# Performance work log

Hardware: AMD Instinct MI355X
Metric: run time of the kernel (lower is better)

## Reference

```python
import jax, jax.numpy as jnp
import numpy as np

D_MODEL = 768
NUM_HEADS = 12
D_K = D_MODEL // NUM_HEADS


def setup_inputs() -> dict:
    key = jax.random.key(0)
    ks = jax.random.split(key, 11)
    B, S = 2, 2048
    s = 1.0 / np.sqrt(D_MODEL)
    inp = {
        'q': jax.random.normal(ks[0], (B, S, D_MODEL), jnp.float32),
        'k': jax.random.normal(ks[1], (B, S, D_MODEL), jnp.float32),
        'v': jax.random.normal(ks[2], (B, S, D_MODEL), jnp.float32),
        'w_q': jax.random.normal(ks[3], (D_MODEL, D_MODEL), jnp.float32) * s,
        'b_q': jnp.zeros((D_MODEL,), jnp.float32),
        'w_k': jax.random.normal(ks[4], (D_MODEL, D_MODEL), jnp.float32) * s,
        'b_k': jnp.zeros((D_MODEL,), jnp.float32),
        'w_v': jax.random.normal(ks[5], (D_MODEL, D_MODEL), jnp.float32) * s,
        'b_v': jnp.zeros((D_MODEL,), jnp.float32),
        'w_o': jax.random.normal(ks[6], (D_MODEL, D_MODEL), jnp.float32) * s,
        'b_o': jnp.zeros((D_MODEL,), jnp.float32),
    }
    return inp


def _split_heads(x):
    # (B, S, D) -> (B, H, S, d_k)
    B, S, _ = x.shape
    return x.reshape(B, S, NUM_HEADS, D_K).transpose(0, 2, 1, 3)


def reference(q, k, v, w_q, b_q, w_k, b_k, w_v, b_v, w_o, b_o):
    qh = _split_heads(q @ w_q + b_q)
    kh = _split_heads(k @ w_k + b_k)
    vh = _split_heads(v @ w_v + b_v)
    scale = 1.0 / jnp.sqrt(jnp.asarray(D_K, qh.dtype))
    scores = jnp.einsum('bhqd,bhkd->bhqk', qh, kh) * scale  # [B,H,Sq,Sk]
    attn_weights = jax.nn.softmax(scores, axis=-1)
    ctx = jnp.einsum('bhqk,bhkd->bhqd', attn_weights, vh)
    B, H, S, _ = ctx.shape
    ctx = ctx.transpose(0, 2, 1, 3).reshape(B, S, D_MODEL)
    out = ctx @ w_o + b_o  # dropout = identity (eval mode)
    return out, attn_weights
```

## Files before the change

### kernel.cpp

```cpp
#include <hip/hip_runtime.h>
#include <math.h>

#define HH 12
#define SS 2048
#define DM 768
#define DK 64

typedef _Float16 f16x8 __attribute__((ext_vector_type(8)));
typedef _Float16 f16x4 __attribute__((ext_vector_type(4)));
typedef float    f32x4 __attribute__((ext_vector_type(4)));

#define MFMA_F16(A, B, C) __builtin_amdgcn_mfma_f32_16x16x32_f16((A), (B), (C), 0, 0, 0)

__global__ __launch_bounds__(256) void conv_w_kernel(
        const float* __restrict__ w0, const float* __restrict__ w1,
        const float* __restrict__ w2, const float* __restrict__ w3,
        _Float16* hi0, _Float16* lo0, _Float16* hi1, _Float16* lo1,
        _Float16* hi2, _Float16* lo2, _Float16* hi3, _Float16* lo3)
{
    __shared__ float T[64][68];
    const int z = blockIdx.z;
    const float* W = (z == 0) ? w0 : (z == 1) ? w1 : (z == 2) ? w2 : w3;
    _Float16* Whi  = (z == 0) ? hi0 : (z == 1) ? hi1 : (z == 2) ? hi2 : hi3;
    _Float16* Wlo  = (z == 0) ? lo0 : (z == 1) ? lo1 : (z == 2) ? lo2 : lo3;

    const int tid = threadIdx.x;
    const int k0 = blockIdx.y * 64, n0 = blockIdx.x * 64;

    #pragma unroll
    for (int i = 0; i < 4; ++i) {
        int r = (tid >> 4) + i * 16;
        int c = (tid & 15) * 4;
        *(float4*)&T[r][c] = *(const float4*)&W[(size_t)(k0 + r) * DM + n0 + c];
    }
    __syncthreads();

    const int n = tid >> 2, kq = (tid & 3) * 16;
    f16x8 ha, la, hb, lb;
    #pragma unroll
    for (int j = 0; j < 8; ++j) {
        float v = T[kq + j][n];
        _Float16 h = (_Float16)v;
        ha[j] = h; la[j] = (_Float16)(v - (float)h);
    }
    #pragma unroll
    for (int j = 0; j < 8; ++j) {
        float v = T[kq + 8 + j][n];
        _Float16 h = (_Float16)v;
        hb[j] = h; lb[j] = (_Float16)(v - (float)h);
    }
    size_t o = (size_t)(n0 + n) * DM + k0 + kq;
    *(f16x8*)&Whi[o]     = ha;
    *(f16x8*)&Whi[o + 8] = hb;
    *(f16x8*)&Wlo[o]     = la;
    *(f16x8*)&Wlo[o + 8] = lb;
}

template <int MODE>
__global__ __launch_bounds__(256) void gemm16_kernel(
        const float* __restrict__ A, const _Float16* __restrict__ Bhi,
        const _Float16* __restrict__ Blo, const float* __restrict__ bias,
        _Float16* __restrict__ Chi, _Float16* __restrict__ Clo,
        float* __restrict__ Cf)
{
    const int tid  = threadIdx.x;
    const int wave = tid >> 6, lane = tid & 63;
    const int lrow = lane & 15;
    const int lk   = (lane >> 4) * 8;
    const int grow = (lane >> 4) * 4;
    const int n0   = blockIdx.x * 64;
    const int m0   = blockIdx.y * 64;
    const int mr   = m0 + wave * 16 + lrow;

    f32x4 acc[4];
    #pragma unroll
    for (int nf = 0; nf < 4; ++nf) acc[nf] = (f32x4){0.f, 0.f, 0.f, 0.f};

    const float* Arow = A + (size_t)mr * DM;

    #pragma unroll 2
    for (int kt = 0; kt < 24; ++kt) {
        const int k0 = kt * 32 + lk;
        float4 x = *(const float4*)&Arow[k0];
        float4 y = *(const float4*)&Arow[k0 + 4];
        float vv[8] = {x.x, x.y, x.z, x.w, y.x, y.y, y.z, y.w};
        f16x8 ah, al;
        #pragma unroll
        for (int j = 0; j < 8; ++j) {
            _Float16 h = (_Float16)vv[j];
            ah[j] = h; al[j] = (_Float16)(vv[j] - (float)h);
        }
        #pragma unroll
        for (int nf = 0; nf < 4; ++nf) {
            const size_t bo = (size_t)(n0 + nf * 16 + lrow) * DM + k0;
            f16x8 bh_ = *(const f16x8*)&Bhi[bo];
            f16x8 bl_ = *(const f16x8*)&Blo[bo];
            acc[nf] = MFMA_F16(ah, bh_, acc[nf]);
            acc[nf] = MFMA_F16(al, bh_, acc[nf]);
            acc[nf] = MFMA_F16(ah, bl_, acc[nf]);
        }
    }

    float bb[4];
    #pragma unroll
    for (int nf = 0; nf < 4; ++nf) bb[nf] = bias[n0 + nf * 16 + lrow];

    if (MODE == 0) {
        const int h = blockIdx.x;
        #pragma unroll
        for (int nf = 0; nf < 4; ++nf)
            #pragma unroll
            for (int r = 0; r < 4; ++r) {
                int m = m0 + wave * 16 + grow + r;
                int b_ = m >> 11, s_ = m & 2047;
                float v = acc[nf][r] + bb[nf];
                _Float16 h16 = (_Float16)v;
                size_t o = (((size_t)(b_ * HH + h) * SS + s_) << 6) + nf * 16 + lrow;
                Chi[o] = h16;
                Clo[o] = (_Float16)(v - (float)h16);
            }
    } else if (MODE == 1) {
        __shared__ _Float16 T[2][64][72];
        #pragma unroll
        for (int nf = 0; nf < 4; ++nf)
            #pragma unroll
            for (int r = 0; r < 4; ++r) {
                float v = acc[nf][r] + bb[nf];
                _Float16 h16 = (_Float16)v;
                int ml = wave * 16 + grow + r;
                T[0][nf * 16 + lrow][ml] = h16;
                T[1][nf * 16 + lrow][ml] = (_Float16)(v - (float)h16);
            }
        __syncthreads();
        const int h  = blockIdx.x;
        const int b_ = m0 >> 11, s0 = m0 & 2047;
        int row = tid >> 1;
        int p = row >> 6, dk = row & 63, sh = (tid & 1) * 32;
        const _Float16* src = &T[p][dk][sh];
        _Float16* dst = (p ? Clo : Chi) +
                        ((size_t)(b_ * HH + h) * DK + dk) * SS + s0 + sh;
        #pragma unroll
        for (int j = 0; j < 32; j += 8)
            *(f16x8*)&dst[j] = *(const f16x8*)&src[j];
    } else {
        #pragma unroll
        for (int nf = 0; nf < 4; ++nf)
            #pragma unroll
            for (int r = 0; r < 4; ++r) {
                int m = m0 + wave * 16 + grow + r;
                Cf[(size_t)m * DM + n0 + nf * 16 + lrow] = acc[nf][r] + bb[nf];
            }
    }
}

__global__ __launch_bounds__(256) void attn_kernel(
        const _Float16* __restrict__ Qhi, const _Float16* __restrict__ Qlo,
        const _Float16* __restrict__ Khi, const _Float16* __restrict__ Klo,
        const _Float16* __restrict__ Vthi, const _Float16* __restrict__ Vtlo,
        float* __restrict__ attnW, float* __restrict__ ctx)
{
    __shared__ float Ps[4][16][34];

    const int tid  = threadIdx.x;
    const int wave = tid >> 6;
    const int lane = tid & 63;
    const int lrow = lane & 15;
    const int lk   = (lane >> 4) * 8;
    const int grow = (lane >> 4) * 4;

    const int qt = blockIdx.x;
    const int bh = blockIdx.y;
    const int qw0 = qt * 64 + wave * 16;
    const size_t qkbase = (size_t)bh * SS * DK;
    const size_t vbase  = (size_t)bh * DK * SS;

    f16x8 qhi[2], qlo[2];
    {
        const size_t qidx = qkbase + (size_t)(qw0 + lrow) * DK + lk;
        qhi[0] = *(const f16x8*)&Qhi[qidx];
        qhi[1] = *(const f16x8*)&Qhi[qidx + 32];
        qlo[0] = *(const f16x8*)&Qlo[qidx];
        qlo[1] = *(const f16x8*)&Qlo[qidx + 32];
    }

    float lsum[4] = {0.f, 0.f, 0.f, 0.f};
    f32x4 Oacc[4];
    #pragma unroll
    for (int n = 0; n < 4; ++n) Oacc[n] = (f32x4){0.f, 0.f, 0.f, 0.f};

    float (*ps)[34] = Ps[wave];

    for (int kt = 0; kt < 64; ++kt) {
        #pragma unroll
        for (int sub = 0; sub < 2; ++sub) {
            const int k16 = kt * 2 + sub;
            const size_t kidx = qkbase + (size_t)(k16 * 16 + lrow) * DK + lk;
            f16x8 khi0 = *(const f16x8*)&Khi[kidx];
            f16x8 khi1 = *(const f16x8*)&Khi[kidx + 32];
            f16x8 klo0 = *(const f16x8*)&Klo[kidx];
            f16x8 klo1 = *(const f16x8*)&Klo[kidx + 32];
            f32x4 cA = {0.f, 0.f, 0.f, 0.f};
            f32x4 cB = {0.f, 0.f, 0.f, 0.f};
            cA = MFMA_F16(qhi[0], khi0, cA);
            cA = MFMA_F16(qhi[1], khi1, cA);
            cA = MFMA_F16(qlo[0], khi0, cA);
            cB = MFMA_F16(qlo[1], khi1, cB);
            cB = MFMA_F16(qhi[0], klo0, cB);
            cB = MFMA_F16(qhi[1], klo1, cB);
            #pragma unroll
            for (int r = 0; r < 4; ++r) {
                float pv = __expf((cA[r] + cB[r]) * 0.125f);
                lsum[r] += pv;
                attnW[((size_t)bh * SS + qw0 + grow + r) * SS + k16 * 16 + lrow] = pv;
                ps[grow + r][sub * 16 + lrow] = pv * 16.0f;
            }
        }
        float pf[8];
        #pragma unroll
        for (int j = 0; j < 8; ++j) pf[j] = ps[lrow][lk + j];
        f16x8 phi, plo;
        #pragma unroll
        for (int j = 0; j < 8; ++j) {
            _Float16 h = (_Float16)pf[j];
            phi[j] = h;
            plo[j] = (_Float16)(pf[j] - (float)h);
        }
        #pragma unroll
        for (int n = 0; n < 4; ++n) {
            const size_t vidx = vbase + (size_t)(n * 16 + lrow) * SS + kt * 32 + lk;
            f16x8 vhi = *(const f16x8*)&Vthi[vidx];
            f16x8 vlo = *(const f16x8*)&Vtlo[vidx];
            Oacc[n] = MFMA_F16(phi, vhi, Oacc[n]);
            Oacc[n] = MFMA_F16(plo, vhi, Oacc[n]);
            Oacc[n] = MFMA_F16(phi, vlo, Oacc[n]);
        }
    }

    #pragma unroll
    for (int r = 0; r < 4; ++r) {
        lsum[r] += __shfl_xor(lsum[r], 1, 64);
        lsum[r] += __shfl_xor(lsum[r], 2, 64);
        lsum[r] += __shfl_xor(lsum[r], 4, 64);
        lsum[r] += __shfl_xor(lsum[r], 8, 64);
    }
    float rl[4];
    #pragma unroll
    for (int r = 0; r < 4; ++r) rl[r] = 1.0f / lsum[r];

    if (lrow == 0) {
        #pragma unroll
        for (int r = 0; r < 4; ++r) ps[grow + r][32] = rl[r];
    }

    for (int r16 = 0; r16 < 16; ++r16) {
        float mrl = ps[r16][32];
        float4* row4 = (float4*)&attnW[((size_t)bh * SS + qw0 + r16) * SS];
        #pragma unroll
        for (int it = 0; it < 8; ++it) {
            float4 vv = row4[it * 64 + lane];
            vv.x *= mrl; vv.y *= mrl; vv.z *= mrl; vv.w *= mrl;
            row4[it * 64 + lane] = vv;
        }
    }

    const int b_ = bh / HH, h_ = bh % HH;
    #pragma unroll
    for (int n = 0; n < 4; ++n)
        #pragma unroll
        for (int r = 0; r < 4; ++r) {
            int q = qw0 + grow + r;
            ctx[((size_t)b_ * SS + q) * DM + h_ * DK + n * 16 + lrow] =
                Oacc[n][r] * rl[r] * 0.0625f;
        }
}

__global__ __launch_bounds__(256) void copy_kernel(
        float* __restrict__ dst, const float* __restrict__ src)
{
    const size_t total4 = (size_t)2 * SS * DM / 4;
    size_t i = (size_t)blockIdx.x * 256 + threadIdx.x;
    const size_t stride = (size_t)gridDim.x * 256;
    float4* d4 = (float4*)dst;
    const float4* s4 = (const float4*)src;
    for (; i < total4; i += stride) d4[i] = s4[i];
}

extern "C" void kernel_launch(void* const* d_in, const int* in_sizes, int n_in,
                              void* d_out, int out_size, void* d_ws, size_t ws_size,
                              hipStream_t stream) {
    const float* q   = (const float*)d_in[0];
    const float* k   = (const float*)d_in[1];
    const float* v   = (const float*)d_in[2];
    const float* w_q = (const float*)d_in[3];
    const float* b_q = (const float*)d_in[4];
    const float* w_k = (const float*)d_in[5];
    const float* b_k = (const float*)d_in[6];
    const float* w_v = (const float*)d_in[7];
    const float* b_v = (const float*)d_in[8];
    const float* w_o = (const float*)d_in[9];
    const float* b_o = (const float*)d_in[10];

    float* out   = (float*)d_out;
    float* attnW = out + (size_t)2 * SS * DM;

    _Float16* wsh = (_Float16*)d_ws;
    const size_t PL = (size_t)2 * HH * SS * DK;
    _Float16* Qhi  = wsh;
    _Float16* Qlo  = wsh + PL;
    _Float16* Khi  = wsh + 2 * PL;
    _Float16* Klo  = wsh + 3 * PL;
    _Float16* Vthi = wsh + 4 * PL;
    _Float16* Vtlo = wsh + 5 * PL;
    float* ctx = (float*)(wsh + 6 * PL);
    float* res = (float*)wsh;

    const size_t WPL = (size_t)DM * DM;
    _Float16* WtQ_hi = (_Float16*)attnW;
    _Float16* WtQ_lo = WtQ_hi + WPL;
    _Float16* WtK_hi = WtQ_hi + 2 * WPL;
    _Float16* WtK_lo = WtQ_hi + 3 * WPL;
    _Float16* WtV_hi = WtQ_hi + 4 * WPL;
    _Float16* WtV_lo = WtQ_hi + 5 * WPL;
    _Float16* WtO_hi = (_Float16*)out;
    _Float16* WtO_lo = WtO_hi + WPL;

    dim3 blk(256);
    conv_w_kernel<<<dim3(12, 12, 4), blk, 0, stream>>>(
        w_q, w_k, w_v, w_o,
        WtQ_hi, WtQ_lo, WtK_hi, WtK_lo, WtV_hi, WtV_lo, WtO_hi, WtO_lo);

    dim3 gg(12, 64);
    gemm16_kernel<0><<<gg, blk, 0, stream>>>(q, WtQ_hi, WtQ_lo, b_q, Qhi, Qlo, nullptr);
    gemm16_kernel<0><<<gg, blk, 0, stream>>>(k, WtK_hi, WtK_lo, b_k, Khi, Klo, nullptr);
    gemm16_kernel<1><<<gg, blk, 0, stream>>>(v, WtV_hi, WtV_lo, b_v, Vthi, Vtlo, nullptr);

    attn_kernel<<<dim3(32, 24), blk, 0, stream>>>(Qhi, Qlo, Khi, Klo, Vthi, Vtlo,
                                                  attnW, ctx);

    gemm16_kernel<2><<<gg, blk, 0, stream>>>(ctx, WtO_hi, WtO_lo, b_o,
                                             nullptr, nullptr, res);

    copy_kernel<<<dim3(1024), blk, 0, stream>>>(out, res);
}
```

Before: 1.317 ms.

## Restructure attention into two-pass softmax with split-K waves and fused QKV GEMM

Attention now makes a first pass that computes only the row sums, then a second pass that writes the already-normalized probabilities straight to attnW. This removes the read-modify-write rescale over the whole attention matrix. Each block splits its keys across two wave pairs and reduces the partial outputs in shared memory. The grid is remapped for locality, and ctx is emitted as hi/lo fp16. Separately, the q/k/v inputs are pre-split to fp16 hi/lo, the three projection GEMMs merge into one launch with coalesced LDS-staged stores, and the output GEMM uses narrower tiles; the cost is that QK^T is computed twice and a split pass is added.

```diff
diff --git a/kernel.cpp b/kernel.cpp
--- a/kernel.cpp
+++ b/kernel.cpp
@@ -11,6 +11,29 @@
 typedef float    f32x4 __attribute__((ext_vector_type(4)));
 
 #define MFMA_F16(A, B, C) __builtin_amdgcn_mfma_f32_16x16x32_f16((A), (B), (C), 0, 0, 0)
+
+__global__ __launch_bounds__(256) void split_a_kernel(
+        const float* __restrict__ q, const float* __restrict__ k,
+        const float* __restrict__ v,
+        _Float16* __restrict__ Ahi, _Float16* __restrict__ Alo)
+{
+    const size_t PER = 786432;
+    size_t f = (size_t)blockIdx.x * 256 + threadIdx.x;
+    int z = (int)(f / PER);
+    size_t loc = f - (size_t)z * PER;
+    const float* src = (z == 0) ? q : (z == 1) ? k : v;
+    float4 x = ((const float4*)src)[loc];
+    float vv[4] = {x.x, x.y, x.z, x.w};
+    f16x4 hi, lo;
+    #pragma unroll
+    for (int j = 0; j < 4; ++j) {
+        _Float16 h = (_Float16)vv[j];
+        hi[j] = h; lo[j] = (_Float16)(vv[j] - (float)h);
+    }
+    size_t off = (size_t)z * 3145728 + loc * 4;
+    *(f16x4*)&Ahi[off] = hi;
+    *(f16x4*)&Alo[off] = lo;
+}
 
 __global__ __launch_bounds__(256) void conv_w_kernel(
         const float* __restrict__ w0, const float* __restrict__ w1,
@@ -56,100 +79,150 @@
     *(f16x8*)&Wlo[o + 8] = lb;
 }
 
-template <int MODE>
-__global__ __launch_bounds__(256) void gemm16_kernel(
-        const float* __restrict__ A, const _Float16* __restrict__ Bhi,
-        const _Float16* __restrict__ Blo, const float* __restrict__ bias,
-        _Float16* __restrict__ Chi, _Float16* __restrict__ Clo,
-        float* __restrict__ Cf)
-{
+__global__ __launch_bounds__(256) void gemm16_qkv_kernel(
+        const _Float16* __restrict__ Ahi, const _Float16* __restrict__ Alo,
+        const _Float16* __restrict__ Wt,
+        const float* __restrict__ b_q, const float* __restrict__ b_k,
+        const float* __restrict__ b_v,
+        _Float16* __restrict__ Qhi, _Float16* __restrict__ Qlo,
+        _Float16* __restrict__ Khi, _Float16* __restrict__ Klo,
+        _Float16* __restrict__ Vthi, _Float16* __restrict__ Vtlo)
+{
+    __shared__ _Float16 T[64][72];
+
     const int tid  = threadIdx.x;
     const int wave = tid >> 6, lane = tid & 63;
     const int lrow = lane & 15;
     const int lk   = (lane >> 4) * 8;
     const int grow = (lane >> 4) * 4;
+    const int z    = blockIdx.z;
     const int n0   = blockIdx.x * 64;
     const int m0   = blockIdx.y * 64;
     const int mr   = m0 + wave * 16 + lrow;
 
-    f32x4 acc[4];
-    #pragma unroll
-    for (int nf = 0; nf < 4; ++nf) acc[nf] = (f32x4){0.f, 0.f, 0.f, 0.f};
-
-    const float* Arow = A + (size_t)mr * DM;
+    const size_t WPL = (size_t)DM * DM;
+    const _Float16* Bhi = Wt + (size_t)z * 2 * WPL;
+    const _Float16* Blo = Bhi + WPL;
+    const float* bias = (z == 0) ? b_q : (z == 1) ? b_k : b_v;
+
+    const _Float16* Ah = Ahi + (size_t)z * 3145728 + (size_t)mr * DM;
+    const _Float16* Al = Alo + (size_t)z * 3145728 + (size_t)mr * DM;
+
+    f32x4 accA[4], accB[4];
+    #pragma unroll
+    for (int nf = 0; nf < 4; ++nf) {
+        accA[nf] = (f32x4){0.f, 0.f, 0.f, 0.f};
+        accB[nf] = (f32x4){0.f, 0.f, 0.f, 0.f};
+    }
 
     #pragma unroll 2
     for (int kt = 0; kt < 24; ++kt) {
         const int k0 = kt * 32 + lk;
-        float4 x = *(const float4*)&Arow[k0];
-        float4 y = *(const float4*)&Arow[k0 + 4];
-        float vv[8] = {x.x, x.y, x.z, x.w, y.x, y.y, y.z, y.w};
-        f16x8 ah, al;
-        #pragma unroll
-        for (int j = 0; j < 8; ++j) {
-            _Float16 h = (_Float16)vv[j];
-            ah[j] = h; al[j] = (_Float16)(vv[j] - (float)h);
-        }
+        f16x8 ah = *(const f16x8*)&Ah[k0];
+        f16x8 al = *(const f16x8*)&Al[k0];
         #pragma unroll
         for (int nf = 0; nf < 4; ++nf) {
             const size_t bo = (size_t)(n0 + nf * 16 + lrow) * DM + k0;
             f16x8 bh_ = *(const f16x8*)&Bhi[bo];
             f16x8 bl_ = *(const f16x8*)&Blo[bo];
-            acc[nf] = MFMA_F16(ah, bh_, acc[nf]);
-            acc[nf] = MFMA_F16(al, bh_, acc[nf]);
-            acc[nf] = MFMA_F16(ah, bl_, acc[nf]);
-        }
-    }
-
-    float bb[4];
-    #pragma unroll
-    for (int nf = 0; nf < 4; ++nf) bb[nf] = bias[n0 + nf * 16 + lrow];
-
-    if (MODE == 0) {
-        const int h = blockIdx.x;
+            accA[nf] = MFMA_F16(ah, bh_, accA[nf]);
+            accB[nf] = MFMA_F16(al, bh_, accB[nf]);
+            accB[nf] = MFMA_F16(ah, bl_, accB[nf]);
+        }
+    }
+
+    _Float16 hi16[4][4], lo16[4][4];
+    #pragma unroll
+    for (int nf = 0; nf < 4; ++nf) {
+        float bb = bias[n0 + nf * 16 + lrow];
+        #pragma unroll
+        for (int r = 0; r < 4; ++r) {
+            float vv = accA[nf][r] + accB[nf][r] + bb;
+            _Float16 h = (_Float16)vv;
+            hi16[nf][r] = h;
+            lo16[nf][r] = (_Float16)(vv - (float)h);
+        }
+    }
+
+    const int head = blockIdx.x;
+    const int b_ = m0 >> 11, s0 = m0 & 2047;
+    _Float16* ChiS = (z == 0) ? Qhi : Khi;
+    _Float16* CloS = (z == 0) ? Qlo : Klo;
+
+    #pragma unroll
+    for (int p = 0; p < 2; ++p) {
+        if (p) __syncthreads();
         #pragma unroll
         for (int nf = 0; nf < 4; ++nf)
             #pragma unroll
             for (int r = 0; r < 4; ++r) {
-                int m = m0 + wave * 16 + grow + r;
-                int b_ = m >> 11, s_ = m & 2047;
-                float v = acc[nf][r] + bb[nf];
-                _Float16 h16 = (_Float16)v;
-                size_t o = (((size_t)(b_ * HH + h) * SS + s_) << 6) + nf * 16 + lrow;
-                Chi[o] = h16;
-                Clo[o] = (_Float16)(v - (float)h16);
-            }
-    } else if (MODE == 1) {
-        __shared__ _Float16 T[2][64][72];
-        #pragma unroll
-        for (int nf = 0; nf < 4; ++nf)
-            #pragma unroll
-            for (int r = 0; r < 4; ++r) {
-                float v = acc[nf][r] + bb[nf];
-                _Float16 h16 = (_Float16)v;
-                int ml = wave * 16 + grow + r;
-                T[0][nf * 16 + lrow][ml] = h16;
-                T[1][nf * 16 + lrow][ml] = (_Float16)(v - (float)h16);
+                _Float16 val = p ? lo16[nf][r] : hi16[nf][r];
+                if (z < 2) T[wave * 16 + grow + r][nf * 16 + lrow] = val;
+                else       T[nf * 16 + lrow][wave * 16 + grow + r] = val;
             }
         __syncthreads();
-        const int h  = blockIdx.x;
-        const int b_ = m0 >> 11, s0 = m0 & 2047;
-        int row = tid >> 1;
-        int p = row >> 6, dk = row & 63, sh = (tid & 1) * 32;
-        const _Float16* src = &T[p][dk][sh];
-        _Float16* dst = (p ? Clo : Chi) +
-                        ((size_t)(b_ * HH + h) * DK + dk) * SS + s0 + sh;
-        #pragma unroll
-        for (int j = 0; j < 32; j += 8)
-            *(f16x8*)&dst[j] = *(const f16x8*)&src[j];
-    } else {
-        #pragma unroll
-        for (int nf = 0; nf < 4; ++nf)
-            #pragma unroll
-            for (int r = 0; r < 4; ++r) {
-                int m = m0 + wave * 16 + grow + r;
-                Cf[(size_t)m * DM + n0 + nf * 16 + lrow] = acc[nf][r] + bb[nf];
-            }
+        int rr = tid >> 2, seg = (tid & 3) * 16;
+        _Float16* dst;
+        if (z < 2)
+            dst = (p ? CloS : ChiS) +
+                  ((size_t)(b_ * HH + head) * SS + s0 + rr) * DK + seg;
+        else
+            dst = (p ? Vtlo : Vthi) +
+                  ((size_t)(b_ * HH + head) * DK + rr) * SS + s0 + seg;
+        *(f16x8*)&dst[0] = *(const f16x8*)&T[rr][seg];
+        *(f16x8*)&dst[8] = *(const f16x8*)&T[rr][seg + 8];
+    }
+}
+
+__global__ __launch_bounds__(256) void gemm16_o_kernel(
+        const _Float16* __restrict__ Ahi, const _Float16* __restrict__ Alo,
+        const _Float16* __restrict__ Bhi, const _Float16* __restrict__ Blo,
+        const float* __restrict__ bias, float* __restrict__ Cf)
+{
+    const int tid  = threadIdx.x;
+    const int wave = tid >> 6, lane = tid & 63;
+    const int lrow = lane & 15;
+    const int lk   = (lane >> 4) * 8;
+    const int grow = (lane >> 4) * 4;
+    const int n0   = blockIdx.x * 32;
+    const int m0   = blockIdx.y * 64;
+    const int mr   = m0 + wave * 16 + lrow;
+
+    const _Float16* Ah = Ahi + (size_t)mr * DM;
+    const _Float16* Al = Alo + (size_t)mr * DM;
+
+    f32x4 accA[2], accB[2];
+    #pragma unroll
+    for (int nf = 0; nf < 2; ++nf) {
+        accA[nf] = (f32x4){0.f, 0.f, 0.f, 0.f};
+        accB[nf] = (f32x4){0.f, 0.f, 0.f, 0.f};
+    }
+
+    #pragma unroll 2
+    for (int kt = 0; kt < 24; ++kt) {
+        const int k0 = kt * 32 + lk;
+        f16x8 ah = *(const f16x8*)&Ah[k0];
+        f16x8 al = *(const f16x8*)&Al[k0];
+        #pragma unroll
+        for (int nf = 0; nf < 2; ++nf) {
+            const size_t bo = (size_t)(n0 + nf * 16 + lrow) * DM + k0;
+            f16x8 bh_ = *(const f16x8*)&Bhi[bo];
+            f16x8 bl_ = *(const f16x8*)&Blo[bo];
+            accA[nf] = MFMA_F16(ah, bh_, accA[nf]);
+            accB[nf] = MFMA_F16(al, bh_, accB[nf]);
+            accB[nf] = MFMA_F16(ah, bl_, accB[nf]);
+        }
+    }
+
+    #pragma unroll
+    for (int nf = 0; nf < 2; ++nf) {
+        float bb = bias[n0 + nf * 16 + lrow];
+        #pragma unroll
+        for (int r = 0; r < 4; ++r) {
+            int m = m0 + wave * 16 + grow + r;
+            Cf[(size_t)m * DM + n0 + nf * 16 + lrow] =
+                accA[nf][r] + accB[nf][r] + bb;
+        }
     }
 }
 
@@ -157,9 +230,12 @@
         const _Float16* __restrict__ Qhi, const _Float16* __restrict__ Qlo,
         const _Float16* __restrict__ Khi, const _Float16* __restrict__ Klo,
         const _Float16* __restrict__ Vthi, const _Float16* __restrict__ Vtlo,
-        float* __restrict__ attnW, float* __restrict__ ctx)
+        float* __restrict__ attnW,
+        _Float16* __restrict__ Chi, _Float16* __restrict__ Clo)
 {
     __shared__ float Ps[4][16][34];
+    __shared__ float Ored[32][68];
+    __shared__ float redL[2][2][16];
 
     const int tid  = threadIdx.x;
     const int wave = tid >> 6;
@@ -167,75 +243,49 @@
     const int lrow = lane & 15;
     const int lk   = (lane >> 4) * 8;
     const int grow = (lane >> 4) * 4;
-
-    const int qt = blockIdx.x;
-    const int bh = blockIdx.y;
-    const int qw0 = qt * 64 + wave * 16;
+    const int qh   = wave >> 1;
+    const int kh   = wave & 1;
+
+    int fid = blockIdx.y * 64 + blockIdx.x;
+    int nid = (fid & 7) * 192 + (fid >> 3);
+    const int qt = nid & 63;
+    const int bh = nid >> 6;
+    const int q0 = qt * 32;
+    const int qw0 = q0 + qh * 16;
+    const int kbase = kh * 1024;
+
     const size_t qkbase = (size_t)bh * SS * DK;
     const size_t vbase  = (size_t)bh * DK * SS;
 
-    f16x8 qhi[2], qlo[2];
+    f16x8 qfh[2], qfl[2];
     {
         const size_t qidx = qkbase + (size_t)(qw0 + lrow) * DK + lk;
-        qhi[0] = *(const f16x8*)&Qhi[qidx];
-        qhi[1] = *(const f16x8*)&Qhi[qidx + 32];
-        qlo[0] = *(const f16x8*)&Qlo[qidx];
-        qlo[1] = *(const f16x8*)&Qlo[qidx + 32];
+        qfh[0] = *(const f16x8*)&Qhi[qidx];
+        qfh[1] = *(const f16x8*)&Qhi[qidx + 32];
+        qfl[0] = *(const f16x8*)&Qlo[qidx];
+        qfl[1] = *(const f16x8*)&Qlo[qidx + 32];
     }
 
     float lsum[4] = {0.f, 0.f, 0.f, 0.f};
-    f32x4 Oacc[4];
-    #pragma unroll
-    for (int n = 0; n < 4; ++n) Oacc[n] = (f32x4){0.f, 0.f, 0.f, 0.f};
-
-    float (*ps)[34] = Ps[wave];
-
-    for (int kt = 0; kt < 64; ++kt) {
-        #pragma unroll
-        for (int sub = 0; sub < 2; ++sub) {
-            const int k16 = kt * 2 + sub;
-            const size_t kidx = qkbase + (size_t)(k16 * 16 + lrow) * DK + lk;
-            f16x8 khi0 = *(const f16x8*)&Khi[kidx];
-            f16x8 khi1 = *(const f16x8*)&Khi[kidx + 32];
-            f16x8 klo0 = *(const f16x8*)&Klo[kidx];
-            f16x8 klo1 = *(const f16x8*)&Klo[kidx + 32];
-            f32x4 cA = {0.f, 0.f, 0.f, 0.f};
-            f32x4 cB = {0.f, 0.f, 0.f, 0.f};
-            cA = MFMA_F16(qhi[0], khi0, cA);
-            cA = MFMA_F16(qhi[1], khi1, cA);
-            cA = MFMA_F16(qlo[0], khi0, cA);
-            cB = MFMA_F16(qlo[1], khi1, cB);
-            cB = MFMA_F16(qhi[0], klo0, cB);
-            cB = MFMA_F16(qhi[1], klo1, cB);
-            #pragma unroll
-            for (int r = 0; r < 4; ++r) {
-                float pv = __expf((cA[r] + cB[r]) * 0.125f);
-                lsum[r] += pv;
-                attnW[((size_t)bh * SS + qw0 + grow + r) * SS + k16 * 16 + lrow] = pv;
-                ps[grow + r][sub * 16 + lrow] = pv * 16.0f;
-            }
-        }
-        float pf[8];
-        #pragma unroll
-        for (int j = 0; j < 8; ++j) pf[j] = ps[lrow][lk + j];
-        f16x8 phi, plo;
-        #pragma unroll
-        for (int j = 0; j < 8; ++j) {
-            _Float16 h = (_Float16)pf[j];
-            phi[j] = h;
-            plo[j] = (_Float16)(pf[j] - (float)h);
-        }
-        #pragma unroll
-        for (int n = 0; n < 4; ++n) {
-            const size_t vidx = vbase + (size_t)(n * 16 + lrow) * SS + kt * 32 + lk;
-            f16x8 vhi = *(const f16x8*)&Vthi[vidx];
-            f16x8 vlo = *(const f16x8*)&Vtlo[vidx];
-            Oacc[n] = MFMA_F16(phi, vhi, Oacc[n]);
-            Oacc[n] = MFMA_F16(plo, vhi, Oacc[n]);
-            Oacc[n] = MFMA_F16(phi, vlo, Oacc[n]);
-        }
-    }
-
+    #pragma unroll 2
+    for (int t = 0; t < 64; ++t) {
+        const size_t kidx = qkbase + (size_t)(kbase + t * 16 + lrow) * DK + lk;
+        f16x8 kh0 = *(const f16x8*)&Khi[kidx];
+        f16x8 kh1 = *(const f16x8*)&Khi[kidx + 32];
+        f16x8 kl0 = *(const f16x8*)&Klo[kidx];
+        f16x8 kl1 = *(const f16x8*)&Klo[kidx + 32];
+        f32x4 cA = {0.f, 0.f, 0.f, 0.f};
+        f32x4 cB = {0.f, 0.f, 0.f, 0.f};
+        cA = MFMA_F16(qfh[0], kh0, cA);
+        cA = MFMA_F16(qfh[1], kh1, cA);
+        cA = MFMA_F16(qfl[0], kh0, cA);
+        cB = MFMA_F16(qfl[1], kh1, cB);
+        cB = MFMA_F16(qfh[0], kl0, cB);
+        cB = MFMA_F16(qfh[1], kl1, cB);
+        #pragma unroll
+        for (int r = 0; r < 4; ++r)
+            lsum[r] += __expf((cA[r] + cB[r]) * 0.125f);
+    }
     #pragma unroll
     for (int r = 0; r < 4; ++r) {
         lsum[r] += __shfl_xor(lsum[r], 1, 64);
@@ -243,35 +293,102 @@
         lsum[r] += __shfl_xor(lsum[r], 4, 64);
         lsum[r] += __shfl_xor(lsum[r], 8, 64);
     }
+    if (lrow == 0) {
+        #pragma unroll
+        for (int r = 0; r < 4; ++r) redL[qh][kh][grow + r] = lsum[r];
+    }
+    __syncthreads();
     float rl[4];
     #pragma unroll
-    for (int r = 0; r < 4; ++r) rl[r] = 1.0f / lsum[r];
-
-    if (lrow == 0) {
-        #pragma unroll
-        for (int r = 0; r < 4; ++r) ps[grow + r][32] = rl[r];
-    }
-
-    for (int r16 = 0; r16 < 16; ++r16) {
-        float mrl = ps[r16][32];
-        float4* row4 = (float4*)&attnW[((size_t)bh * SS + qw0 + r16) * SS];
-        #pragma unroll
-        for (int it = 0; it < 8; ++it) {
-            float4 vv = row4[it * 64 + lane];
-            vv.x *= mrl; vv.y *= mrl; vv.z *= mrl; vv.w *= mrl;
-            row4[it * 64 + lane] = vv;
-        }
-    }
+    for (int r = 0; r < 4; ++r)
+        rl[r] = 1.0f / (redL[qh][0][grow + r] + redL[qh][1][grow + r]);
+
+    f32x4 Oacc[4];
+    #pragma unroll
+    for (int n = 0; n < 4; ++n) Oacc[n] = (f32x4){0.f, 0.f, 0.f, 0.f};
+
+    float (*ps)[34] = Ps[wave];
+
+    for (int kc = 0; kc < 32; ++kc) {
+        #pragma unroll
+        for (int sub = 0; sub < 2; ++sub) {
+            const int key0 = kbase + kc * 32 + sub * 16;
+            const size_t kidx = qkbase + (size_t)(key0 + lrow) * DK + lk;
+            f16x8 kh0 = *(const f16x8*)&Khi[kidx];
+            f16x8 kh1 = *(const f16x8*)&Khi[kidx + 32];
+            f16x8 kl0 = *(const f16x8*)&Klo[kidx];
+            f16x8 kl1 = *(const f16x8*)&Klo[kidx + 32];
+            f32x4 cA = {0.f, 0.f, 0.f, 0.f};
+            f32x4 cB = {0.f, 0.f, 0.f, 0.f};
+            cA = MFMA_F16(qfh[0], kh0, cA);
+            cA = MFMA_F16(qfh[1], kh1, cA);
+            cA = MFMA_F16(qfl[0], kh0, cA);
+            cB = MFMA_F16(qfl[1], kh1, cB);
+            cB = MFMA_F16(qfh[0], kl0, cB);
+            cB = MFMA_F16(qfh[1], kl1, cB);
+            #pragma unroll
+            for (int r = 0; r < 4; ++r) {
+                float p = __expf((cA[r] + cB[r]) * 0.125f) * rl[r];
+                attnW[((size_t)bh * SS + qw0 + grow + r) * SS + key0 + lrow] = p;
+                ps[grow + r][sub * 16 + lrow] = p * 256.0f;
+            }
+        }
+        float pf[8];
+        #pragma unroll
+        for (int j = 0; j < 8; ++j) pf[j] = ps[lrow][lk + j];
+        f16x8 ph, pl;
+        #pragma unroll
+        for (int j = 0; j < 8; ++j) {
+            _Float16 h = (_Float16)pf[j];
+            ph[j] = h;
+            pl[j] = (_Float16)(pf[j] - (float)h);
+        }
+        #pragma unroll
+        for (int n = 0; n < 4; ++n) {
+            const size_t vidx = vbase + (size_t)(n * 16 + lrow) * SS +
+                                kbase + kc * 32 + lk;
+            f16x8 vh = *(const f16x8*)&Vthi[vidx];
+            f16x8 vl = *(const f16x8*)&Vtlo[vidx];
+            Oacc[n] = MFMA_F16(ph, vh, Oacc[n]);
+            Oacc[n] = MFMA_F16(pl, vh, Oacc[n]);
+            Oacc[n] = MFMA_F16(ph, vl, Oacc[n]);
+        }
+    }
+
+    __syncthreads();
+    if (kh == 0) {
+        #pragma unroll
+        for (int n = 0; n < 4; ++n)
+            #pragma unroll
+            for (int r = 0; r < 4; ++r)
+                Ored[qh * 16 + grow + r][n * 16 + lrow] = Oacc[n][r];
+    }
+    __syncthreads();
+    if (kh == 1) {
+        #pragma unroll
+        for (int n = 0; n < 4; ++n)
+            #pragma unroll
+            for (int r = 0; r < 4; ++r)
+                Ored[qh * 16 + grow + r][n * 16 + lrow] += Oacc[n][r];
+    }
+    __syncthreads();
 
     const int b_ = bh / HH, h_ = bh % HH;
     #pragma unroll
-    for (int n = 0; n < 4; ++n)
-        #pragma unroll
-        for (int r = 0; r < 4; ++r) {
-            int q = qw0 + grow + r;
-            ctx[((size_t)b_ * SS + q) * DM + h_ * DK + n * 16 + lrow] =
-                Oacc[n][r] * rl[r] * 0.0625f;
-        }
+    for (int it = 0; it < 2; ++it) {
+        int row = (tid >> 4) + it * 16;
+        int c4  = (tid & 15) * 4;
+        f16x4 hi, lo;
+        #pragma unroll
+        for (int j = 0; j < 4; ++j) {
+            float vv = Ored[row][c4 + j] * 0.00390625f;
+            _Float16 h = (_Float16)vv;
+            hi[j] = h; lo[j] = (_Float16)(vv - (float)h);
+        }
+        size_t co = ((size_t)b_ * SS + q0 + row) * DM + h_ * DK + c4;
+        *(f16x4*)&Chi[co] = hi;
+        *(f16x4*)&Clo[co] = lo;
+    }
 }
 
 __global__ __launch_bounds__(256) void copy_kernel(
@@ -305,40 +422,38 @@
 
     _Float16* wsh = (_Float16*)d_ws;
     const size_t PL = (size_t)2 * HH * SS * DK;
-    _Float16* Qhi  = wsh;
-    _Float16* Qlo  = wsh + PL;
-    _Float16* Khi  = wsh + 2 * PL;
-    _Float16* Klo  = wsh + 3 * PL;
-    _Float16* Vthi = wsh + 4 * PL;
-    _Float16* Vtlo = wsh + 5 * PL;
-    float* ctx = (float*)(wsh + 6 * PL);
+    _Float16* Qhi   = wsh;
+    _Float16* Qlo   = wsh + PL;
+    _Float16* Khi   = wsh + 2 * PL;
+    _Float16* Klo   = wsh + 3 * PL;
+    _Float16* Vthi  = wsh + 4 * PL;
+    _Float16* Vtlo  = wsh + 5 * PL;
+    _Float16* ctxhi = wsh + 6 * PL;
+    _Float16* ctxlo = wsh + 7 * PL;
     float* res = (float*)wsh;
 
     const size_t WPL = (size_t)DM * DM;
-    _Float16* WtQ_hi = (_Float16*)attnW;
-    _Float16* WtQ_lo = WtQ_hi + WPL;
-    _Float16* WtK_hi = WtQ_hi + 2 * WPL;
-    _Float16* WtK_lo = WtQ_hi + 3 * WPL;
-    _Float16* WtV_hi = WtQ_hi + 4 * WPL;
-    _Float16* WtV_lo = WtQ_hi + 5 * WPL;
+    _Float16* Wt   = (_Float16*)attnW;
+    _Float16* AhiP = Wt + 6 * WPL;
+    _Float16* AloP = AhiP + 3 * PL;
     _Float16* WtO_hi = (_Float16*)out;
     _Float16* WtO_lo = WtO_hi + WPL;
 
     dim3 blk(256);
+    split_a_kernel<<<dim3(9216), blk, 0, stream>>>(q, k, v, AhiP, AloP);
     conv_w_kernel<<<dim3(12, 12, 4), blk, 0, stream>>>(
         w_q, w_k, w_v, w_o,
-        WtQ_hi, WtQ_lo, WtK_hi, WtK_lo, WtV_hi, WtV_lo, WtO_hi, WtO_lo);
-
-    dim3 gg(12, 64);
-    gemm16_kernel<0><<<gg, blk, 0, stream>>>(q, WtQ_hi, WtQ_lo, b_q, Qhi, Qlo, nullptr);
-    gemm16_kernel<0><<<gg, blk, 0, stream>>>(k, WtK_hi, WtK_lo, b_k, Khi, Klo, nullptr);
-    gemm16_kernel<1><<<gg, blk, 0, stream>>>(v, WtV_hi, WtV_lo, b_v, Vthi, Vtlo, nullptr);
-
-    attn_kernel<<<dim3(32, 24), blk, 0, stream>>>(Qhi, Qlo, Khi, Klo, Vthi, Vtlo,
-                                                  attnW, ctx);
-
-    gemm16_kernel<2><<<gg, blk, 0, stream>>>(ctx, WtO_hi, WtO_lo, b_o,
-                                             nullptr, nullptr, res);
+        Wt, Wt + WPL, Wt + 2 * WPL, Wt + 3 * WPL, Wt + 4 * WPL, Wt + 5 * WPL,
+        WtO_hi, WtO_lo);
+
+    gemm16_qkv_kernel<<<dim3(12, 64, 3), blk, 0, stream>>>(
+        AhiP, AloP, Wt, b_q, b_k, b_v, Qhi, Qlo, Khi, Klo, Vthi, Vtlo);
+
+    attn_kernel<<<dim3(64, 24), blk, 0, stream>>>(
+        Qhi, Qlo, Khi, Klo, Vthi, Vtlo, attnW, ctxhi, ctxlo);
+
+    gemm16_o_kernel<<<dim3(24, 64), blk, 0, stream>>>(
+        ctxhi, ctxlo, WtO_hi, WtO_lo, b_o, res);
 
     copy_kernel<<<dim3(1024), blk, 0, stream>>>(out, res);
 }
```

Result: slower. 1.366 ms (+3.7%).
